# Kernel tuning notes

Hardware: AMD Instinct MI355X
Metric: run time of the kernel (lower is better)

Reference implementation:

```python
import jax, jax.numpy as jnp
import numpy as np

B, S, D, H = 4, 2048, 768, 12
HD = D // H  # head_dim = 64
NEG = 1e10
EPS = 1e-5

def setup_inputs() -> dict:
    key = jax.random.key(0)
    k1, k2, k3 = jax.random.split(key, 3)
    return {
        "context": jax.random.normal(k1, (B, S, D), dtype=jnp.float32),
        "pad_mask": jnp.ones((B, S), dtype=jnp.float32),
        "w_qkv": jax.random.normal(k2, (D, 3 * D), dtype=jnp.float32) * 0.02,
        "w_proj": jax.random.normal(k3, (D, D), dtype=jnp.float32) * (0.02 / np.sqrt(2.0 * 12)),
        "b_proj": jnp.zeros((D,), dtype=jnp.float32),
        "gamma": jnp.ones((D,), dtype=jnp.float32),
        "beta": jnp.zeros((D,), dtype=jnp.float32),
    }

def reference(context, pad_mask, w_qkv, w_proj, b_proj, gamma, beta):
    b, s, d = context.shape
    resid = context
    qkv = context @ w_qkv                       # [B,S,3D]
    q, k, v = jnp.split(qkv, 3, axis=-1)
    # [B,S,D] -> [B,H,S,HD]
    q = q.reshape(b, s, H, HD).transpose(0, 2, 1, 3)
    k = k.reshape(b, s, H, HD).transpose(0, 2, 1, 3)
    v = v.reshape(b, s, H, HD).transpose(0, 2, 1, 3)
    scores = jnp.einsum("bhqd,bhkd->bhqk", q, k) * (1.0 / np.sqrt(HD))
    m = pad_mask[:, None, None, :]              # [B,1,1,S]
    scores = scores * m - (1.0 - m) * NEG       # multiplicative mask + big negative
    attn = jax.nn.softmax(scores, axis=-1)      # dropout is identity at inference
    out = jnp.einsum("bhqk,bhkd->bhqd", attn, v)
    out = out.transpose(0, 2, 1, 3).reshape(b, s, d)
    out = out @ w_proj + b_proj
    x = out + resid
    mu = jnp.mean(x, axis=-1, keepdims=True)
    var = jnp.var(x, axis=-1, keepdims=True)
    return (x - mu) * jax.lax.rsqrt(var + EPS) * gamma + beta
```

## Files before the change

### kernel.cpp

```cpp
#include <hip/hip_runtime.h>

#define BB 4
#define SS 2048
#define DD 768
#define HH 12
#define HDD 64
#define BS (BB*SS)
#define NQKV (3*DD)
#define NEL (BS*DD)

typedef __attribute__((ext_vector_type(8))) __bf16 bf16x8;
typedef __attribute__((ext_vector_type(4))) float fx4;
typedef __attribute__((ext_vector_type(4))) int   ix4;

#define MFMA16(a,b,c) __builtin_amdgcn_mfma_f32_16x16x32_bf16((a),(b),(c),0,0,0)

#define GLLDS(g, l) __builtin_amdgcn_global_load_lds( \
    (const __attribute__((address_space(1))) void*)(g), \
    (__attribute__((address_space(3))) void*)(l), 16, 0, 0)

__device__ __forceinline__ unsigned short f2bf(float f) {
  unsigned u = __builtin_bit_cast(unsigned, f);
  u = (u + 0x7FFFu + ((u >> 16) & 1u)) >> 16;
  return (unsigned short)u;
}
__device__ __forceinline__ unsigned pkbf(float a, float b) {
  unsigned ua = __builtin_bit_cast(unsigned, a);
  unsigned ub = __builtin_bit_cast(unsigned, b);
  return ((ua + 0x8000u) >> 16) | ((ub + 0x8000u) & 0xFFFF0000u);
}
__device__ __forceinline__ unsigned cvtpk(float a, float b) {
  unsigned r;
  asm("v_cvt_pk_bf16_f32 %0, %1, %2" : "=v"(r) : "v"(a), "v"(b));
  return r;
}
__device__ __forceinline__ float ex2(float x) { return __builtin_amdgcn_exp2f(x); }

__global__ __launch_bounds__(256) void pack_bf16(const float* __restrict__ x,
                                                 unsigned short* __restrict__ y, int n4) {
  int i = blockIdx.x * 256 + threadIdx.x;
  if (i < n4) {
    float4 v = ((const float4*)x)[i];
    ((uint2*)y)[i] = make_uint2(pkbf(v.x, v.y), pkbf(v.z, v.w));
  }
}

__global__ __launch_bounds__(256) void mask_coef_k(const float* __restrict__ m,
                                                   float* __restrict__ ka,
                                                   float* __restrict__ kb, int n) {
  int i = blockIdx.x * 256 + threadIdx.x;
  if (i < n) {
    float v = m[i];
    ka[i] = v * 0.18033688f;
    kb[i] = __builtin_fmaf(v, 1.44269504e10f, -1.44269504e10f);
  }
}

__global__ __launch_bounds__(256) void pack_transpose(const float* __restrict__ w,
                                                      unsigned short* __restrict__ wT,
                                                      int K, int N) {
  __shared__ unsigned short t[32][33];
  int n0 = blockIdx.x * 32, k0 = blockIdx.y * 32;
  int tx = threadIdx.x & 31, ty = threadIdx.x >> 5;
#pragma unroll
  for (int r = ty; r < 32; r += 8)
    t[tx][r] = f2bf(w[(size_t)(k0 + r) * N + n0 + tx]);
  __syncthreads();
#pragma unroll
  for (int r = ty; r < 32; r += 8)
    wT[(size_t)(n0 + r) * K + k0 + tx] = t[r][tx];
}

__global__ __launch_bounds__(256) void gemm_qkv_k(const unsigned short* __restrict__ Wt,
                                                  const unsigned short* __restrict__ X,
                                                  unsigned short* __restrict__ Qo,
                                                  unsigned short* __restrict__ Ko,
                                                  unsigned short* __restrict__ Vto) {
  __shared__ unsigned short As[2 * 128 * 32];
  __shared__ unsigned short Bs[2 * 128 * 32];
  const int tid = threadIdx.x;
  const int w = tid >> 6, lane = tid & 63, quad = lane >> 4, l16 = lane & 15;
  const int m0 = blockIdx.y << 7;
  const int n0 = blockIdx.x << 7;
  const int wm = (w & 1) * 64, wn = (w >> 1) * 64;
  fx4 acc[4][4];
#pragma unroll
  for (int i = 0; i < 4; ++i)
#pragma unroll
    for (int c = 0; c < 4; ++c) acc[i][c] = (fx4){0.f, 0.f, 0.f, 0.f};

  const int c0 = tid, c1 = 256 + tid;
  const unsigned short* Ag0 = Wt + (size_t)(m0 + (c0 >> 2)) * DD + (c0 & 3) * 8;
  const unsigned short* Ag1 = Wt + (size_t)(m0 + (c1 >> 2)) * DD + (c1 & 3) * 8;
  const unsigned short* Bg0 = X + (size_t)(n0 + (c0 >> 2)) * DD + (c0 & 3) * 8;
  const unsigned short* Bg1 = X + (size_t)(n0 + (c1 >> 2)) * DD + (c1 & 3) * 8;
  const int wb = w * 1024;

  GLLDS(Ag0, (char*)As + wb);
  GLLDS(Ag1, (char*)As + 4096 + wb);
  GLLDS(Bg0, (char*)Bs + wb);
  GLLDS(Bg1, (char*)Bs + 4096 + wb);
  int cur = 0;

  for (int k0 = 0; k0 < DD; k0 += 32) {
    __syncthreads();
    if (k0 + 32 < DD) {
      GLLDS(Ag0 + k0 + 32, (char*)As + (cur ^ 1) * 8192 + wb);
      GLLDS(Ag1 + k0 + 32, (char*)As + (cur ^ 1) * 8192 + 4096 + wb);
      GLLDS(Bg0 + k0 + 32, (char*)Bs + (cur ^ 1) * 8192 + wb);
      GLLDS(Bg1 + k0 + 32, (char*)Bs + (cur ^ 1) * 8192 + 4096 + wb);
    }
    const unsigned short* Asc = As + cur * 4096;
    const unsigned short* Bsc = Bs + cur * 4096;
    bf16x8 af[4], bf[4];
#pragma unroll
    for (int i = 0; i < 4; ++i) af[i] = *(const bf16x8*)&Asc[(wm + i * 16 + l16) * 32 + quad * 8];
#pragma unroll
    for (int c = 0; c < 4; ++c) bf[c] = *(const bf16x8*)&Bsc[(wn + c * 16 + l16) * 32 + quad * 8];
#pragma unroll
    for (int i = 0; i < 4; ++i)
#pragma unroll
      for (int c = 0; c < 4; ++c) acc[i][c] = MFMA16(af[i], bf[c], acc[i][c]);
    cur ^= 1;
  }

  const int which = m0 / DD;
#pragma unroll
  for (int i = 0; i < 4; ++i) {
    int fb = m0 + wm + i * 16 + quad * 4;
    int d = fb - which * DD;
    int h = d >> 6, hd = d & 63;
#pragma unroll
    for (int c = 0; c < 4; ++c) {
      int srow = n0 + wn + c * 16 + l16;
      int b = srow >> 11, s = srow & (SS - 1);
      if (which == 0) {
        uint2 v = make_uint2(pkbf(acc[i][c][0], acc[i][c][1]), pkbf(acc[i][c][2], acc[i][c][3]));
        *(uint2*)&Qo[((size_t)(b * HH + h) * SS + s) * HDD + hd] = v;
      } else if (which == 1) {
        uint2 v = make_uint2(pkbf(acc[i][c][0], acc[i][c][1]), pkbf(acc[i][c][2], acc[i][c][3]));
        *(uint2*)&Ko[((size_t)(b * HH + h) * SS + s) * HDD + hd] = v;
      } else {
#pragma unroll
        for (int r = 0; r < 4; ++r)
          Vto[((size_t)(b * HH + h) * HDD + hd + r) * SS + s] = f2bf(acc[i][c][r]);
      }
    }
  }
}

__global__ __launch_bounds__(256) void gemm_proj_k(const unsigned short* __restrict__ Wt,
                                                   const unsigned short* __restrict__ X,
                                                   const float* __restrict__ ctx,
                                                   const float* __restrict__ bproj,
                                                   float* __restrict__ xf) {
  __shared__ unsigned short As[2 * 128 * 32];
  __shared__ unsigned short Bs[2 * 128 * 32];
  const int tid = threadIdx.x;
  const int w = tid >> 6, lane = tid & 63, quad = lane >> 4, l16 = lane & 15;
  const int m0 = blockIdx.y << 7;
  const int n0 = blockIdx.x << 7;
  const int wm = (w & 1) * 64, wn = (w >> 1) * 64;
  fx4 acc[4][4];
#pragma unroll
  for (int i = 0; i < 4; ++i)
#pragma unroll
    for (int c = 0; c < 4; ++c) acc[i][c] = (fx4){0.f, 0.f, 0.f, 0.f};

  const int c0 = tid, c1 = 256 + tid;
  const unsigned short* Ag0 = Wt + (size_t)(m0 + (c0 >> 2)) * DD + (c0 & 3) * 8;
  const unsigned short* Ag1 = Wt + (size_t)(m0 + (c1 >> 2)) * DD + (c1 & 3) * 8;
  const unsigned short* Bg0 = X + (size_t)(n0 + (c0 >> 2)) * DD + (c0 & 3) * 8;
  const unsigned short* Bg1 = X + (size_t)(n0 + (c1 >> 2)) * DD + (c1 & 3) * 8;
  const int wb = w * 1024;

  GLLDS(Ag0, (char*)As + wb);
  GLLDS(Ag1, (char*)As + 4096 + wb);
  GLLDS(Bg0, (char*)Bs + wb);
  GLLDS(Bg1, (char*)Bs + 4096 + wb);
  int cur = 0;

  for (int k0 = 0; k0 < DD; k0 += 32) {
    __syncthreads();
    if (k0 + 32 < DD) {
      GLLDS(Ag0 + k0 + 32, (char*)As + (cur ^ 1) * 8192 + wb);
      GLLDS(Ag1 + k0 + 32, (char*)As + (cur ^ 1) * 8192 + 4096 + wb);
      GLLDS(Bg0 + k0 + 32, (char*)Bs + (cur ^ 1) * 8192 + wb);
      GLLDS(Bg1 + k0 + 32, (char*)Bs + (cur ^ 1) * 8192 + 4096 + wb);
    }
    const unsigned short* Asc = As + cur * 4096;
    const unsigned short* Bsc = Bs + cur * 4096;
    bf16x8 af[4], bf[4];
#pragma unroll
    for (int i = 0; i < 4; ++i) af[i] = *(const bf16x8*)&Asc[(wm + i * 16 + l16) * 32 + quad * 8];
#pragma unroll
    for (int c = 0; c < 4; ++c) bf[c] = *(const bf16x8*)&Bsc[(wn + c * 16 + l16) * 32 + quad * 8];
#pragma unroll
    for (int i = 0; i < 4; ++i)
#pragma unroll
      for (int c = 0; c < 4; ++c) acc[i][c] = MFMA16(af[i], bf[c], acc[i][c]);
    cur ^= 1;
  }

#pragma unroll
  for (int i = 0; i < 4; ++i) {
    int fb = m0 + wm + i * 16 + quad * 4;
    float4 bp = *(const float4*)&bproj[fb];
#pragma unroll
    for (int c = 0; c < 4; ++c) {
      int srow = n0 + wn + c * 16 + l16;
      float4 cx = *(const float4*)&ctx[(size_t)srow * DD + fb];
      float4 r;
      r.x = acc[i][c][0] + bp.x + cx.x;
      r.y = acc[i][c][1] + bp.y + cx.y;
      r.z = acc[i][c][2] + bp.z + cx.z;
      r.w = acc[i][c][3] + bp.w + cx.w;
      *(float4*)&xf[(size_t)srow * DD + fb] = r;
    }
  }
}

__global__ __launch_bounds__(256) void attn_k(const unsigned short* __restrict__ Q,
                                              const unsigned short* __restrict__ K,
                                              const unsigned short* __restrict__ Vt,
                                              const float* __restrict__ ka,
                                              const float* __restrict__ kb,
                                              unsigned short* __restrict__ O) {
  __shared__ unsigned short Ks[2 * 64 * 64];
  __shared__ unsigned short Vts[2 * 64 * 64];
  const int tid = threadIdx.x;
  const int w = tid >> 6, lane = tid & 63;
  const int quad = lane >> 4, l16 = lane & 15;
  const int bh = blockIdx.y;
  const int b = bh / HH, h = bh - b * HH;
  const int q0 = blockIdx.x << 7;
  const unsigned short* Qb = Q + (size_t)bh * (SS * HDD);
  const unsigned short* Kb = K + (size_t)bh * (SS * HDD);
  const unsigned short* Vtb = Vt + (size_t)bh * (SS * HDD);
  const float* ka_b = ka + b * SS;
  const float* kb_b = kb + b * SS;

  bf16x8 qf[2][2];
#pragma unroll
  for (int qi = 0; qi < 2; ++qi)
#pragma unroll
    for (int f = 0; f < 2; ++f)
      qf[qi][f] = *(const bf16x8*)&Qb[(size_t)(q0 + w * 32 + qi * 16 + l16) * HDD + f * 32 + quad * 8];

  fx4 o[2][4];
#pragma unroll
  for (int qi = 0; qi < 2; ++qi)
#pragma unroll
    for (int ht = 0; ht < 4; ++ht) o[qi][ht] = (fx4){0.f, 0.f, 0.f, 0.f};
  fx4 sacc[2];
  sacc[0] = (fx4){0.f, 0.f, 0.f, 0.f};
  sacc[1] = (fx4){0.f, 0.f, 0.f, 0.f};

  const ix4 one4 = (ix4){0x3F803F80, 0x3F803F80, 0x3F803F80, 0x3F803F80};
  const bf16x8 onesf = __builtin_bit_cast(bf16x8, one4);

  const int cA = tid, cB = 256 + tid;
  const int rA = cA >> 3, pA = (cA & 7) ^ (rA & 7);
  const int rB = cB >> 3, pB = (cB & 7) ^ (rB & 7);
  const unsigned short* kSrcA = Kb + (size_t)rA * HDD + pA * 8;
  const unsigned short* kSrcB = Kb + (size_t)rB * HDD + pB * 8;
  const unsigned short* vSrcA = Vtb + (size_t)rA * SS + pA * 8;
  const unsigned short* vSrcB = Vtb + (size_t)rB * SS + pB * 8;
  const int wbA = w * 1024;
  const int wbB = 4096 + w * 1024;

  GLLDS(kSrcA, (char*)Ks + wbA);
  GLLDS(kSrcB, (char*)Ks + wbB);
  GLLDS(vSrcA, (char*)Vts + wbA);
  GLLDS(vSrcB, (char*)Vts + wbB);
  int cur = 0;

  for (int k0 = 0; k0 < SS; k0 += 64) {
    __syncthreads();
    if (k0 + 64 < SS) {
      int kn = k0 + 64;
      GLLDS(kSrcA + (size_t)kn * HDD, (char*)Ks + (cur ^ 1) * 8192 + wbA);
      GLLDS(kSrcB + (size_t)kn * HDD, (char*)Ks + (cur ^ 1) * 8192 + wbB);
      GLLDS(vSrcA + kn, (char*)Vts + (cur ^ 1) * 8192 + wbA);
      GLLDS(vSrcB + kn, (char*)Vts + (cur ^ 1) * 8192 + wbB);
    }
    const unsigned short* Ksc = Ks + cur * 4096;
    const char* Vtsc = (const char*)Vts + cur * 8192;

    float4 mqa[4], mqb[4];
#pragma unroll
    for (int kt = 0; kt < 4; ++kt) {
      mqa[kt] = *(const float4*)&ka_b[k0 + kt * 16 + quad * 4];
      mqb[kt] = *(const float4*)&kb_b[k0 + kt * 16 + quad * 4];
    }

    bf16x8 kf[4][2];
#pragma unroll
    for (int kt = 0; kt < 4; ++kt) {
      int row = kt * 16 + l16;
      int rx = row & 7;
#pragma unroll
      for (int f = 0; f < 2; ++f)
        kf[kt][f] = *(const bf16x8*)&Ksc[row * 64 + ((f * 4 + quad) ^ rx) * 8];
    }
    bf16x8 vf[4][2];
#pragma unroll
    for (int ht = 0; ht < 4; ++ht) {
      int row = ht * 16 + l16;
      int rx = row & 7;
#pragma unroll
      for (int f = 0; f < 2; ++f) {
        int dc0 = (f * 4 + (quad >> 1)) ^ rx;
        int dc1 = (f * 4 + 2 + (quad >> 1)) ^ rx;
        uint2 lo = *(const uint2*)(Vtsc + row * 128 + dc0 * 16 + (quad & 1) * 8);
        uint2 hi = *(const uint2*)(Vtsc + row * 128 + dc1 * 16 + (quad & 1) * 8);
        ix4 vv = (ix4){(int)lo.x, (int)lo.y, (int)hi.x, (int)hi.y};
        vf[ht][f] = __builtin_bit_cast(bf16x8, vv);
      }
    }

    __builtin_amdgcn_s_setprio(1);
#pragma unroll
    for (int qi = 0; qi < 2; ++qi) {
      unsigned pw[8];
#pragma unroll
      for (int kt = 0; kt < 4; ++kt) {
        fx4 s = (fx4){0.f, 0.f, 0.f, 0.f};
        s = MFMA16(kf[kt][0], qf[qi][0], s);
        s = MFMA16(kf[kt][1], qf[qi][1], s);
        const float* ma = (const float*)&mqa[kt];
        const float* mc = (const float*)&mqb[kt];
        float p0 = ex2(__builtin_fmaf(s[0], ma[0], mc[0]));
        float p1 = ex2(__builtin_fmaf(s[1], ma[1], mc[1]));
        float p2 = ex2(__builtin_fmaf(s[2], ma[2], mc[2]));
        float p3 = ex2(__builtin_fmaf(s[3], ma[3], mc[3]));
        pw[kt * 2]     = cvtpk(p0, p1);
        pw[kt * 2 + 1] = cvtpk(p2, p3);
      }
      ix4 pi0 = (ix4){(int)pw[0], (int)pw[1], (int)pw[2], (int)pw[3]};
      ix4 pi1 = (ix4){(int)pw[4], (int)pw[5], (int)pw[6], (int)pw[7]};
      bf16x8 pf0 = __builtin_bit_cast(bf16x8, pi0);
      bf16x8 pf1 = __builtin_bit_cast(bf16x8, pi1);
      sacc[qi] = MFMA16(onesf, pf0, sacc[qi]);
      sacc[qi] = MFMA16(onesf, pf1, sacc[qi]);
#pragma unroll
      for (int ht = 0; ht < 4; ++ht) {
        o[qi][ht] = MFMA16(vf[ht][0], pf0, o[qi][ht]);
        o[qi][ht] = MFMA16(vf[ht][1], pf1, o[qi][ht]);
      }
    }
    __builtin_amdgcn_s_setprio(0);
    cur ^= 1;
  }

#pragma unroll
  for (int qi = 0; qi < 2; ++qi) {
    float inv = 1.f / fmaxf(sacc[qi][0], 1e-30f);
    int sq = q0 + w * 32 + qi * 16 + l16;
    unsigned short* orow = O + ((size_t)(b * SS + sq)) * DD + h * HDD;
#pragma unroll
    for (int ht = 0; ht < 4; ++ht) {
      uint2 v = make_uint2(pkbf(o[qi][ht][0] * inv, o[qi][ht][1] * inv),
                           pkbf(o[qi][ht][2] * inv, o[qi][ht][3] * inv));
      *(uint2*)&orow[ht * 16 + quad * 4] = v;
    }
  }
}

__global__ __launch_bounds__(256) void ln_k(const float* __restrict__ x,
                                            const float* __restrict__ gamma,
                                            const float* __restrict__ beta,
                                            float* __restrict__ out) {
  const int row = blockIdx.x;
  const float* xr = x + (size_t)row * DD;
  const int t = threadIdx.x;
  float v0 = xr[t], v1 = xr[t + 256], v2 = xr[t + 512];
  float s = v0 + v1 + v2;
  float ss = v0 * v0 + v1 * v1 + v2 * v2;
#pragma unroll
  for (int d = 32; d > 0; d >>= 1) {
    s += __shfl_down(s, d);
    ss += __shfl_down(ss, d);
  }
  __shared__ float sh[10];
  int wv = t >> 6, lane = t & 63;
  if (lane == 0) { sh[wv] = s; sh[4 + wv] = ss; }
  __syncthreads();
  if (t == 0) {
    float S = sh[0] + sh[1] + sh[2] + sh[3];
    float SSm = sh[4] + sh[5] + sh[6] + sh[7];
    float mu = S * (1.0f / DD);
    float var = SSm * (1.0f / DD) - mu * mu;
    sh[8] = mu;
    sh[9] = rsqrtf(var + 1e-5f);
  }
  __syncthreads();
  float mu = sh[8], rstd = sh[9];
  out[(size_t)row * DD + t]       = (v0 - mu) * rstd * gamma[t]       + beta[t];
  out[(size_t)row * DD + t + 256] = (v1 - mu) * rstd * gamma[t + 256] + beta[t + 256];
  out[(size_t)row * DD + t + 512] = (v2 - mu) * rstd * gamma[t + 512] + beta[t + 512];
}

extern "C" void kernel_launch(void* const* d_in, const int* in_sizes, int n_in,
                              void* d_out, int out_size, void* d_ws, size_t ws_size,
                              hipStream_t stream) {
  (void)in_sizes; (void)n_in; (void)out_size; (void)ws_size;
  const float* ctx   = (const float*)d_in[0];
  const float* mask  = (const float*)d_in[1];
  const float* wqkv  = (const float*)d_in[2];
  const float* wproj = (const float*)d_in[3];
  const float* bproj = (const float*)d_in[4];
  const float* gamma = (const float*)d_in[5];
  const float* beta  = (const float*)d_in[6];
  float* out = (float*)d_out;

  char* p = (char*)d_ws;
  unsigned short* Xbf = (unsigned short*)p; p += (size_t)NEL * 2;
  unsigned short* Qw  = (unsigned short*)p; p += (size_t)NEL * 2;
  unsigned short* Kw  = (unsigned short*)p; p += (size_t)NEL * 2;
  unsigned short* Vtw = (unsigned short*)p; p += (size_t)NEL * 2;
  unsigned short* Ao  = (unsigned short*)p; p += (size_t)NEL * 2;
  unsigned short* WqkvT  = (unsigned short*)p; p += (size_t)DD * NQKV * 2;
  unsigned short* WprojT = (unsigned short*)p; p += (size_t)DD * DD * 2;
  float* kaw = (float*)p; p += (size_t)BS * 4;
  float* kbw = (float*)p; p += (size_t)BS * 4;
  float* xf = (float*)Qw;

  pack_bf16<<<NEL / 4 / 256, 256, 0, stream>>>(ctx, Xbf, NEL / 4);
  mask_coef_k<<<BS / 256, 256, 0, stream>>>(mask, kaw, kbw, BS);
  pack_transpose<<<dim3(NQKV / 32, DD / 32), 256, 0, stream>>>(wqkv, WqkvT, DD, NQKV);
  pack_transpose<<<dim3(DD / 32, DD / 32), 256, 0, stream>>>(wproj, WprojT, DD, DD);
  gemm_qkv_k<<<dim3(BS / 128, NQKV / 128), 256, 0, stream>>>(WqkvT, Xbf, Qw, Kw, Vtw);
  attn_k<<<dim3(SS / 128, BB * HH), 256, 0, stream>>>(Qw, Kw, Vtw, kaw, kbw, Ao);
  gemm_proj_k<<<dim3(BS / 128, DD / 128), 256, 0, stream>>>(WprojT, Ao, ctx, bproj, xf);
  ln_k<<<BS, 256, 0, stream>>>(xf, gamma, beta, out);
}
```

Baseline: 277.7 us.

## Stage K/V tiles via registers into single LDS buffer, cache mask in LDS

Replaces the double-buffered direct global-to-LDS K/V prefetch with register prefetch of the next tile, written into a single LDS buffer between two barriers each iteration. Per-batch mask coefficients ka/kb are copied into shared memory once per block instead of being read from global memory every tile. The s_setprio hints are removed. This halves K/V LDS use but adds 16KB of mask storage and an extra barrier per iteration, and the register staging adds VGPR pressure.

```diff
diff --git a/kernel.cpp b/kernel.cpp
--- a/kernel.cpp
+++ b/kernel.cpp
@@ -226,8 +226,10 @@
                                               const float* __restrict__ ka,
                                               const float* __restrict__ kb,
                                               unsigned short* __restrict__ O) {
-  __shared__ unsigned short Ks[2 * 64 * 64];
-  __shared__ unsigned short Vts[2 * 64 * 64];
+  __shared__ unsigned short Ks[64 * 64];
+  __shared__ unsigned short Vts[64 * 64];
+  __shared__ float kaS[SS];
+  __shared__ float kbS[SS];
   const int tid = threadIdx.x;
   const int w = tid >> 6, lane = tid & 63;
   const int quad = lane >> 4, l16 = lane & 15;
@@ -240,6 +242,13 @@
   const float* ka_b = ka + b * SS;
   const float* kb_b = kb + b * SS;
 
+#pragma unroll
+  for (int i = 0; i < 2; ++i) {
+    int idx = i * 256 + tid;
+    ((float4*)kaS)[idx] = ((const float4*)ka_b)[idx];
+    ((float4*)kbS)[idx] = ((const float4*)kb_b)[idx];
+  }
+
   bf16x8 qf[2][2];
 #pragma unroll
   for (int qi = 0; qi < 2; ++qi)
@@ -262,36 +271,32 @@
   const int cA = tid, cB = 256 + tid;
   const int rA = cA >> 3, pA = (cA & 7) ^ (rA & 7);
   const int rB = cB >> 3, pB = (cB & 7) ^ (rB & 7);
-  const unsigned short* kSrcA = Kb + (size_t)rA * HDD + pA * 8;
-  const unsigned short* kSrcB = Kb + (size_t)rB * HDD + pB * 8;
-  const unsigned short* vSrcA = Vtb + (size_t)rA * SS + pA * 8;
-  const unsigned short* vSrcB = Vtb + (size_t)rB * SS + pB * 8;
-  const int wbA = w * 1024;
-  const int wbB = 4096 + w * 1024;
-
-  GLLDS(kSrcA, (char*)Ks + wbA);
-  GLLDS(kSrcB, (char*)Ks + wbB);
-  GLLDS(vSrcA, (char*)Vts + wbA);
-  GLLDS(vSrcB, (char*)Vts + wbB);
-  int cur = 0;
+
+  ix4 rk0 = *(const ix4*)&Kb[(size_t)rA * HDD + pA * 8];
+  ix4 rk1 = *(const ix4*)&Kb[(size_t)rB * HDD + pB * 8];
+  ix4 rv0 = *(const ix4*)&Vtb[(size_t)rA * SS + pA * 8];
+  ix4 rv1 = *(const ix4*)&Vtb[(size_t)rB * SS + pB * 8];
 
   for (int k0 = 0; k0 < SS; k0 += 64) {
+    __syncthreads();
+    *(ix4*)((char*)Ks + cA * 16) = rk0;
+    *(ix4*)((char*)Ks + cB * 16) = rk1;
+    *(ix4*)((char*)Vts + cA * 16) = rv0;
+    *(ix4*)((char*)Vts + cB * 16) = rv1;
     __syncthreads();
     if (k0 + 64 < SS) {
       int kn = k0 + 64;
-      GLLDS(kSrcA + (size_t)kn * HDD, (char*)Ks + (cur ^ 1) * 8192 + wbA);
-      GLLDS(kSrcB + (size_t)kn * HDD, (char*)Ks + (cur ^ 1) * 8192 + wbB);
-      GLLDS(vSrcA + kn, (char*)Vts + (cur ^ 1) * 8192 + wbA);
-      GLLDS(vSrcB + kn, (char*)Vts + (cur ^ 1) * 8192 + wbB);
-    }
-    const unsigned short* Ksc = Ks + cur * 4096;
-    const char* Vtsc = (const char*)Vts + cur * 8192;
+      rk0 = *(const ix4*)&Kb[(size_t)(kn + rA) * HDD + pA * 8];
+      rk1 = *(const ix4*)&Kb[(size_t)(kn + rB) * HDD + pB * 8];
+      rv0 = *(const ix4*)&Vtb[(size_t)rA * SS + kn + pA * 8];
+      rv1 = *(const ix4*)&Vtb[(size_t)rB * SS + kn + pB * 8];
+    }
 
     float4 mqa[4], mqb[4];
 #pragma unroll
     for (int kt = 0; kt < 4; ++kt) {
-      mqa[kt] = *(const float4*)&ka_b[k0 + kt * 16 + quad * 4];
-      mqb[kt] = *(const float4*)&kb_b[k0 + kt * 16 + quad * 4];
+      mqa[kt] = *(const float4*)&kaS[k0 + kt * 16 + quad * 4];
+      mqb[kt] = *(const float4*)&kbS[k0 + kt * 16 + quad * 4];
     }
 
     bf16x8 kf[4][2];
@@ -301,7 +306,7 @@
       int rx = row & 7;
 #pragma unroll
       for (int f = 0; f < 2; ++f)
-        kf[kt][f] = *(const bf16x8*)&Ksc[row * 64 + ((f * 4 + quad) ^ rx) * 8];
+        kf[kt][f] = *(const bf16x8*)&Ks[row * 64 + ((f * 4 + quad) ^ rx) * 8];
     }
     bf16x8 vf[4][2];
 #pragma unroll
@@ -312,14 +317,13 @@
       for (int f = 0; f < 2; ++f) {
         int dc0 = (f * 4 + (quad >> 1)) ^ rx;
         int dc1 = (f * 4 + 2 + (quad >> 1)) ^ rx;
-        uint2 lo = *(const uint2*)(Vtsc + row * 128 + dc0 * 16 + (quad & 1) * 8);
-        uint2 hi = *(const uint2*)(Vtsc + row * 128 + dc1 * 16 + (quad & 1) * 8);
+        uint2 lo = *(const uint2*)((const char*)Vts + row * 128 + dc0 * 16 + (quad & 1) * 8);
+        uint2 hi = *(const uint2*)((const char*)Vts + row * 128 + dc1 * 16 + (quad & 1) * 8);
         ix4 vv = (ix4){(int)lo.x, (int)lo.y, (int)hi.x, (int)hi.y};
         vf[ht][f] = __builtin_bit_cast(bf16x8, vv);
       }
     }
 
-    __builtin_amdgcn_s_setprio(1);
 #pragma unroll
     for (int qi = 0; qi < 2; ++qi) {
       unsigned pw[8];
@@ -349,8 +353,6 @@
         o[qi][ht] = MFMA16(vf[ht][1], pf1, o[qi][ht]);
       }
     }
-    __builtin_amdgcn_s_setprio(0);
-    cur ^= 1;
   }
 
 #pragma unroll
```

Result: faster. 252.3 us (-9.2%).
